# Performance work log

Measured on AMD Instinct MI355X. Metric: run time of the kernel, lower is better.

## Reference

```python
import jax, jax.numpy as jnp
import numpy as np

TAU = 10.0          # tau_init
R_MAX = 8           # max(groupconvs)
GROUPCONVS = (4, 8)
PADS = (0, 8)       # (k - spat_red)//2 for k in (17, 33), spat_red = 33 - 2*8 = 17
NEG_SLOPE = 0.01    # LeakyReLU default


def lrelu(t):
    return jnp.where(t >= 0, t, NEG_SLOPE * t)


def rotate_kernel(w, theta):
    """Rotate square kernels w:[N,k,k] by theta, matching torch
    F.affine_grid + F.grid_sample (bilinear, zero padding, align_corners=False)."""
    N, k, _ = w.shape
    coords = (2.0 * jnp.arange(k) + 1.0) / k - 1.0  # normalized pixel centers
    gy, gx = jnp.meshgrid(coords, coords, indexing='ij')
    c, s = jnp.cos(theta), jnp.sin(theta)
    sx = c * gx - s * gy
    sy = s * gx + c * gy
    fx = ((sx + 1.0) * k - 1.0) / 2.0
    fy = ((sy + 1.0) * k - 1.0) / 2.0
    x0 = jnp.floor(fx).astype(jnp.int32)
    y0 = jnp.floor(fy).astype(jnp.int32)
    wf = w.reshape(N, k * k)

    def gather(yi, xi):
        valid = ((yi >= 0) & (yi < k) & (xi >= 0) & (xi < k)).astype(w.dtype)
        idx = jnp.clip(yi, 0, k - 1) * k + jnp.clip(xi, 0, k - 1)
        return wf[:, idx.reshape(-1)].reshape(N, k, k) * valid

    wx1 = fx - x0
    wy1 = fy - y0
    return (gather(y0, x0) * (1 - wy1) * (1 - wx1)
            + gather(y0, x0 + 1) * (1 - wy1) * wx1
            + gather(y0 + 1, x0) * wy1 * (1 - wx1)
            + gather(y0 + 1, x0 + 1) * wy1 * wx1)


def group_conv(x, w, b, pad):
    """GroupConv with input_rot_dim=1: x [B,1,H,W], w [O,1,1,k,k] -> [B,O,R_MAX,H',W']."""
    O, k = w.shape[0], w.shape[-1]
    w2 = w.reshape(O, k, k)
    angles = (2.0 * jnp.pi / R_MAX) * jnp.arange(R_MAX)
    tw = jax.vmap(lambda th: rotate_kernel(w2, th))(angles)   # [R,O,k,k]
    tw = jnp.transpose(tw, (1, 0, 2, 3)).reshape(O * R_MAX, 1, k, k)
    y = jax.lax.conv_general_dilated(x, tw, (1, 1), [(pad, pad), (pad, pad)],
                                     dimension_numbers=('NCHW', 'OIHW', 'NCHW'))
    B, _, H, W = y.shape
    return y.reshape(B, O, R_MAX, H, W) + b[None, :, None, None, None]


def conv1x1(h, w, b):
    # 1x1x1 Conv3d: h [B,C,R,H,W], w [O,C], b [O]
    return jnp.einsum('bcrhw,oc->borhw', h, w) + b[None, :, None, None, None]


def scatter_sum(outs, weights, axis):
    """slice_scatter-based alignment: embed smaller-rdim tensors into the
    largest one at stride max_dim//dim, weight, and sum."""
    max_out = outs[-1]
    md = max_out.shape[axis]
    total = max_out * weights[-1]
    for i, o in enumerate(outs[:-1]):
        step = md // o.shape[axis]
        idx = tuple(slice(None, None, step) if a == axis else slice(None)
                    for a in range(max_out.ndim))
        total = total + jnp.zeros_like(max_out).at[idx].set(o) * weights[i]
    return total


OFFSETS = np.array([0, np.pi / 4, np.pi / 2, 3 * np.pi / 4, np.pi,
                    -3 * np.pi / 4, -np.pi / 2, -np.pi / 4], dtype=np.float32)


def _forward(x, ksize_weight, rdim_weight, conv1_w0, conv1_b0, conv1_w1, conv1_b1,
             conv2_w, conv2_b, conva_w, conva_b, convz_w, convz_b,
             g_ksize, g_rdim, g_attn):
    # gumbel-softmax over kernel sizes (soft, tau=TAU)
    alphas = jax.nn.softmax((ksize_weight + g_ksize) / TAU)
    x_out = (alphas[0] * lrelu(group_conv(x, conv1_w0, conv1_b0, PADS[0]))
             + alphas[1] * lrelu(group_conv(x, conv1_w1, conv1_b1, PADS[1])))
    xs_out = [x_out[:, :, ::R_MAX // r] for r in GROUPCONVS]
    hs = [lrelu(conv1x1(xo, conv2_w[i], conv2_b[i])) for i, xo in enumerate(xs_out)]
    attns = [conv1x1(h, conva_w[i], conva_b[i])[:, 0] for i, h in enumerate(hs)]
    betas = jax.nn.softmax((rdim_weight + g_rdim) / TAU)
    attn = scatter_sum(attns, betas, axis=1)          # [B,R,H,W]
    offsets = jnp.asarray(OFFSETS)
    sigma = np.pi  # theta_prior; Normal(0, sigma) log-prob at offsets
    p_r = (-0.5 * (offsets / sigma) ** 2 - np.float32(np.log(sigma))
           - np.float32(0.5 * np.log(2.0 * np.pi)))[:, None, None]
    attn = attn + p_r
    B = attn.shape[0]
    flat = attn.reshape(B, -1)
    q_t_r = jax.nn.log_softmax(flat, axis=1).reshape(attn.shape)
    # F.gumbel_softmax(a, dim=-1) with default tau=1
    a_sampled = jax.nn.softmax(flat + g_attn, axis=-1).reshape(attn.shape)
    zs = [conv1x1(h, convz_w[i], convz_b[i]) for i, h in enumerate(hs)]
    z = scatter_sum(zs, betas, axis=2)                # [B,2L,R,H,W]
    # faithful to source: `thetas = [c_r(h) for c_r, h in zip(self.conv_z, hs)]`
    # reuses conv_z, so pre-refinement theta == z
    theta_pre = z
    rotation_offset = jnp.broadcast_to(offsets[None, :, None, None], a_sampled.shape)
    theta = jnp.stack((theta_pre[:, 0] + rotation_offset, theta_pre[:, 1]), axis=1)
    return attn, q_t_r, p_r, a_sampled, offsets, theta, z


def setup_inputs() -> dict:
    key = jax.random.key(0)
    ks = jax.random.split(key, 16)
    B, n, KN, L = 8, 64, 128, 2
    gum = lambda k, shape: -jnp.log(-jnp.log(
        jax.random.uniform(k, shape, jnp.float32, 1e-10, 1.0)))
    return {
        'x': jax.random.normal(ks[0], (B, 1, n, n), jnp.float32),
        'ksize_weight': 0.001 * jax.random.normal(ks[1], (2,), jnp.float32),
        'rdim_weight': 0.001 * jax.random.normal(ks[2], (2,), jnp.float32),
        'conv1_w0': 0.02 * jax.random.normal(ks[3], (KN, 1, 1, 17, 17), jnp.float32),
        'conv1_b0': 0.01 * jax.random.normal(ks[4], (KN,), jnp.float32),
        'conv1_w1': 0.02 * jax.random.normal(ks[5], (KN, 1, 1, 33, 33), jnp.float32),
        'conv1_b1': 0.01 * jax.random.normal(ks[6], (KN,), jnp.float32),
        'conv2_w': (1.0 / np.sqrt(KN)) * jax.random.normal(ks[7], (2, KN, KN), jnp.float32),
        'conv2_b': 0.01 * jax.random.normal(ks[8], (2, KN), jnp.float32),
        'conva_w': (1.0 / np.sqrt(KN)) * jax.random.normal(ks[9], (2, 1, KN), jnp.float32),
        'conva_b': 0.01 * jax.random.normal(ks[10], (2, 1), jnp.float32),
        'convz_w': (1.0 / np.sqrt(KN)) * jax.random.normal(ks[11], (2, 2 * L, KN), jnp.float32),
        'convz_b': 0.01 * jax.random.normal(ks[12], (2, 2 * L), jnp.float32),
        'g_ksize': gum(ks[13], (2,)),
        'g_rdim': gum(ks[14], (2,)),
        'g_attn': gum(ks[15], (B, R_MAX * 48 * 48)),
    }


def reference(x, ksize_weight, rdim_weight, conv1_w0, conv1_b0, conv1_w1, conv1_b1,
              conv2_w, conv2_b, conva_w, conva_b, convz_w, convz_b,
              g_ksize, g_rdim, g_attn):
    return _forward(x, ksize_weight, rdim_weight, conv1_w0, conv1_b0, conv1_w1,
                    conv1_b1, conv2_w, conv2_b, conva_w, conva_b, convz_w, convz_b,
                    g_ksize, g_rdim, g_attn)
```

## Files before the change

### kernel.cpp

```cpp
#include <hip/hip_runtime.h>
#include <hip/hip_bf16.h>
#include <math.h>

#define PI_D 3.14159265358979323846

typedef __attribute__((ext_vector_type(8))) short bf16x8;
typedef __attribute__((ext_vector_type(4))) float f32x4;
typedef __attribute__((ext_vector_type(4))) unsigned int u32x4;

#define OFF_SCAL   0u
#define OFF_W2B    4u
#define OFF_BF     16388u
#define OFF_XOUTB  917508u
#define OFF_A0     10354692u
#define OFF_A1     10428420u
#define OFF_Z0     10575876u
#define OFF_Z1     10870788u

#define NS33 42
#define NS17 13

__device__ __forceinline__ float off_r(int r) {
  int m = (r <= 4) ? r : r - 8;
  return (float)(PI_D / 4.0) * (float)m;
}
__device__ __forceinline__ float lrelu_f(float v) { return (v >= 0.f) ? v : 0.01f * v; }
__device__ __forceinline__ short f2bf(float f) {
  __bf16 h = (__bf16)f;
  return __builtin_bit_cast(short, h);
}

__global__ void k_prep(const float* __restrict__ kw, const float* __restrict__ gk,
                       const float* __restrict__ rw, const float* __restrict__ gr,
                       const float* __restrict__ w0, const float* __restrict__ w1,
                       const float* __restrict__ w2, float* __restrict__ scal,
                       short* __restrict__ w2b, short* __restrict__ bfrag) {
  int t = blockIdx.x * blockDim.x + threadIdx.x;
  if (t == 0) {
    float a0 = (kw[0] + gk[0]) * 0.1f, a1 = (kw[1] + gk[1]) * 0.1f;
    float m = fmaxf(a0, a1);
    float e0 = expf(a0 - m), e1 = expf(a1 - m), inv = 1.f / (e0 + e1);
    scal[0] = e0 * inv; scal[1] = e1 * inv;
    float b0 = (rw[0] + gr[0]) * 0.1f, b1 = (rw[1] + gr[1]) * 0.1f;
    m = fmaxf(b0, b1);
    e0 = expf(b0 - m); e1 = expf(b1 - m); inv = 1.f / (e0 + e1);
    scal[2] = e0 * inv; scal[3] = e1 * inv;
  }
  if (t < 2 * 128 * 128) w2b[t] = f2bf(w2[t]);
  int o = t & 127;
  int q = t >> 7;
  int kb = q & 3; q >>= 2;
  int c = q % 55; int r = q / 55;
  float theta = (float)(PI_D / 4.0) * (float)r;
  float cth = cosf(theta), sth = sinf(theta);
  short out[8];
#pragma unroll
  for (int j = 0; j < 8; ++j) {
    float val = 0.f;
    int kk, k, dy, dx;
    const float* wsrc;
    if (c < NS33) { kk = 32 * c + 8 * kb + j; k = 33; dy = kk / 40; dx = kk - 40 * dy; wsrc = w1; }
    else          { kk = 32 * (c - NS33) + 8 * kb + j; k = 17; dy = kk / 24; dx = kk - 24 * dy; wsrc = w0; }
    if (dy < k && dx < k) {
      int kk2 = k * k;
      const float* wo = wsrc + o * kk2;
      float cy = (2.0f * (float)dy + 1.0f) / (float)k - 1.0f;
      float cx = (2.0f * (float)dx + 1.0f) / (float)k - 1.0f;
      float sx = cth * cx - sth * cy;
      float sy = sth * cx + cth * cy;
      float fx = ((sx + 1.0f) * (float)k - 1.0f) * 0.5f;
      float fy = ((sy + 1.0f) * (float)k - 1.0f) * 0.5f;
      float x0f = floorf(fx), y0f = floorf(fy);
      int x0 = (int)x0f, y0 = (int)y0f;
      float wx1 = fx - x0f, wy1 = fy - y0f;
      float acc = 0.f;
#define CORNER(Y, X, CW) { int yy = (Y), xx = (X); \
      if (yy >= 0 && yy < k && xx >= 0 && xx < k) acc += wo[yy * k + xx] * (CW); }
      CORNER(y0,     x0,     (1.f - wy1) * (1.f - wx1));
      CORNER(y0,     x0 + 1, (1.f - wy1) * wx1);
      CORNER(y0 + 1, x0,     wy1 * (1.f - wx1));
      CORNER(y0 + 1, x0 + 1, wy1 * wx1);
#undef CORNER
      val = acc;
    }
    out[j] = f2bf(val);
  }
  *(bf16x8*)(bfrag + (size_t)t * 8) =
      (bf16x8){out[0], out[1], out[2], out[3], out[4], out[5], out[6], out[7]};
}

#define TDW 3080
#define SHW 1544
__global__ __launch_bounds__(256, 4) void k_conv_mfma(
    const float* __restrict__ x, const short* __restrict__ bfrag,
    const float* __restrict__ b17, const float* __restrict__ b33,
    const float* __restrict__ scal, short* __restrict__ xoutb) {
  __shared__ unsigned int lds[SHW + 1540];
  unsigned short* lA = (unsigned short*)lds;
  unsigned short* lB = (unsigned short*)(lds + SHW);
  int blk = blockIdx.x;
  int pt = blk % 36; int t2 = blk / 36; int r = t2 & 7, b = t2 >> 3;
  int p0 = pt * 64;
  int ybase = p0 / 48;
  int tid = threadIdx.x;
  for (int idx = tid; idx < TDW; idx += 256) {
    int ty = idx / 88, tx = idx - ty * 88;
    int gy = ybase + ty - 8, gx = tx - 8;
    float v = 0.f;
    if (gy >= 0 && gy < 64 && gx >= 0 && gx < 64) v = x[(b * 64 + gy) * 64 + gx];
    unsigned short h = (unsigned short)f2bf(v);
    lA[idx] = h;
    if (idx > 0) lB[idx - 1] = h;
  }
  if (tid == 0) lB[TDW - 1] = 0;
  __syncthreads();

  int lane = tid & 63, w = tid >> 6;
  int wm = w >> 1, wn = w & 1;
  int kc = lane >> 4;
  int ln = lane & 15;
  int mloc[2];
#pragma unroll
  for (int mf = 0; mf < 2; ++mf) {
    int p = p0 + wm * 32 + mf + 2 * ln;
    int ym = p / 48, xm = p - ym * 48;
    mloc[mf] = (ym - ybase) * 88 + xm;
  }
  const short* bb = bfrag + (size_t)r * (55 * 4 * 128 * 8);
  int nb0 = wn * 64;

  f32x4 acc33[2][4];
#pragma unroll
  for (int mf = 0; mf < 2; ++mf)
#pragma unroll
    for (int nf = 0; nf < 4; ++nf) acc33[mf][nf] = (f32x4){0.f, 0.f, 0.f, 0.f};

#define LOADB(dst, cg)                                                          \
  {                                                                             \
    _Pragma("unroll")                                                           \
    for (int nf = 0; nf < 4; ++nf)                                              \
      dst[nf] = *(const bf16x8*)(bb + ((size_t)((cg)*4 + kc) * 128 + nb0 + nf * 16 + ln) * 8); \
  }
#define READA(dst, mf, vv)                                                      \
  {                                                                             \
    int bd_ = ((vv) >> 1) + ((mf) ? SHW : 0);                                   \
    u32x4 uv_ = {lds[bd_], lds[bd_ + 1], lds[bd_ + 2], lds[bd_ + 3]};           \
    dst = __builtin_bit_cast(bf16x8, uv_);                                      \
  }

  {
    int dxb = 8 * kc;
    int off = dxb;
    bf16x8 bc[4], bn[4];
    LOADB(bc, 0);
    for (int c = 0; c < NS33; ++c) {
      if (c + 1 < NS33) LOADB(bn, c + 1);
      bf16x8 a0, a1;
      READA(a0, 0, mloc[0] + off);
      READA(a1, 1, mloc[1] + off);
#pragma unroll
      for (int nf = 0; nf < 4; ++nf) {
        acc33[0][nf] = __builtin_amdgcn_mfma_f32_16x16x32_bf16(a0, bc[nf], acc33[0][nf], 0, 0, 0);
        acc33[1][nf] = __builtin_amdgcn_mfma_f32_16x16x32_bf16(a1, bc[nf], acc33[1][nf], 0, 0, 0);
      }
#pragma unroll
      for (int nf = 0; nf < 4; ++nf) bc[nf] = bn[nf];
      int nd = dxb + 32;
      int wr = (nd >= 40);
      dxb = wr ? nd - 40 : nd;
      off += wr ? 80 : 32;
    }
  }

  f32x4 acc17[2][4];
#pragma unroll
  for (int mf = 0; mf < 2; ++mf)
#pragma unroll
    for (int nf = 0; nf < 4; ++nf) acc17[mf][nf] = (f32x4){0.f, 0.f, 0.f, 0.f};
  {
    int t8 = 8 * kc;
    int dy0 = t8 / 24;
    int dxb = t8 - 24 * dy0;
    int off = (8 + dy0) * 88 + 8 + dxb;
    for (int c = 0; c < NS17; ++c) {
      bf16x8 bc[4];
      LOADB(bc, NS33 + c);
      bf16x8 a0, a1;
      READA(a0, 0, mloc[0] + off);
      READA(a1, 1, mloc[1] + off);
#pragma unroll
      for (int nf = 0; nf < 4; ++nf) {
        acc17[0][nf] = __builtin_amdgcn_mfma_f32_16x16x32_bf16(a0, bc[nf], acc17[0][nf], 0, 0, 0);
        acc17[1][nf] = __builtin_amdgcn_mfma_f32_16x16x32_bf16(a1, bc[nf], acc17[1][nf], 0, 0, 0);
      }
      int nd = dxb + 8;
      int wr = (nd >= 24);
      dxb = wr ? nd - 24 : nd;
      off += wr ? 160 : 96;
    }
  }
#undef LOADB
#undef READA

  float a0s = scal[0], a1s = scal[1];
  int dq = lane >> 4;
#pragma unroll
  for (int nf = 0; nf < 4; ++nf) {
    int n = nb0 + nf * 16 + ln;
    float bb17 = b17[n], bb33 = b33[n];
#pragma unroll
    for (int mf = 0; mf < 2; ++mf) {
#pragma unroll
      for (int i = 0; i < 4; ++i) {
        int m = wm * 32 + mf + 8 * dq + 2 * i;
        float v = a0s * lrelu_f(acc17[mf][nf][i] + bb17)
                + a1s * lrelu_f(acc33[mf][nf][i] + bb33);
        xoutb[((size_t)(b * 8 + r) * 2304 + p0 + m) * 128 + n] = f2bf(v);
      }
    }
  }
}

__global__ __launch_bounds__(256, 8) void k_pw_mfma(
    const short* __restrict__ xoutb, const short* __restrict__ w2b_,
    const float* __restrict__ b2_, const float* __restrict__ wa_,
    const float* __restrict__ ba_, const float* __restrict__ wz_,
    const float* __restrict__ bz_,
    float* __restrict__ a0buf, float* __restrict__ z0buf,
    float* __restrict__ a1buf, float* __restrict__ z1buf) {
  __shared__ float sA[64];
  __shared__ float sZ[4][64];
  int blk = blockIdx.x;
  int i1 = (blk >= 1152);
  int lblk = i1 ? blk - 1152 : blk;
  int nR = i1 ? 8 : 4, rstep = i1 ? 1 : 2;
  const short* w2b = w2b_ + (i1 ? 128 * 128 : 0);
  const float* b2 = b2_ + (i1 ? 128 : 0);
  const float* wa = wa_ + (i1 ? 128 : 0);
  const float* ba = ba_ + i1;
  const float* wz = wz_ + (i1 ? 512 : 0);
  const float* bz = bz_ + (i1 ? 4 : 0);
  float* attn_out = i1 ? a1buf : a0buf;
  float* z_out = i1 ? z1buf : z0buf;

  int pblk = lblk % 36;
  int t = lblk / 36;
  int rl = t % nR;
  int b = t / nR;
  int pix0 = pblk * 64;
  int tid = threadIdx.x;
  int lane = tid & 63, w = tid >> 6;
  int kc = lane >> 4, ln = lane & 15;
  int pwave = pix0 + w * 16;
  const short* arow = xoutb + ((size_t)(b * 8 + rl * rstep) * 2304 + pwave) * 128;

  f32x4 acc[8];
#pragma unroll
  for (int nf = 0; nf < 8; ++nf) acc[nf] = (f32x4){0.f, 0.f, 0.f, 0.f};
#pragma unroll
  for (int s = 0; s < 4; ++s) {
    bf16x8 a = *(const bf16x8*)(arow + ln * 128 + s * 32 + kc * 8);
#pragma unroll
    for (int nf = 0; nf < 8; ++nf) {
      bf16x8 bv = *(const bf16x8*)(w2b + (nf * 16 + ln) * 128 + s * 32 + kc * 8);
      acc[nf] = __builtin_amdgcn_mfma_f32_16x16x32_bf16(a, bv, acc[nf], 0, 0, 0);
    }
  }

  float attn_acc[4] = {0.f, 0.f, 0.f, 0.f};
  float zacc[4][4];
#pragma unroll
  for (int j = 0; j < 4; ++j)
#pragma unroll
    for (int q = 0; q < 4; ++q) zacc[j][q] = 0.f;
#pragma unroll
  for (int nf = 0; nf < 8; ++nf) {
    int n = nf * 16 + ln;
    float bb2 = b2[n];
    float wan = wa[n];
    float wz0 = wz[n], wz1 = wz[128 + n], wz2 = wz[256 + n], wz3 = wz[384 + n];
#pragma unroll
    for (int q = 0; q < 4; ++q) {
      float h = lrelu_f(acc[nf][q] + bb2);
      attn_acc[q] = fmaf(wan, h, attn_acc[q]);
      zacc[0][q] = fmaf(wz0, h, zacc[0][q]);
      zacc[1][q] = fmaf(wz1, h, zacc[1][q]);
      zacc[2][q] = fmaf(wz2, h, zacc[2][q]);
      zacc[3][q] = fmaf(wz3, h, zacc[3][q]);
    }
  }
#pragma unroll
  for (int off = 1; off < 16; off <<= 1) {
#pragma unroll
    for (int q = 0; q < 4; ++q) {
      attn_acc[q] += __shfl_xor(attn_acc[q], off);
#pragma unroll
      for (int j = 0; j < 4; ++j) zacc[j][q] += __shfl_xor(zacc[j][q], off);
    }
  }
  if (ln == 0) {
    float ba0 = ba[0];
#pragma unroll
    for (int q = 0; q < 4; ++q) {
      int px = w * 16 + kc * 4 + q;
      sA[px] = attn_acc[q] + ba0;
#pragma unroll
      for (int j = 0; j < 4; ++j) sZ[j][px] = zacc[j][q] + bz[j];
    }
  }
  __syncthreads();
  int px = tid & 63, jj = tid >> 6;
  if (jj == 0)
    attn_out[((size_t)b * nR + rl) * 2304 + pix0 + px] = sA[px];
  z_out[(((size_t)b * 4 + jj) * nR + rl) * 2304 + pix0 + px] = sZ[jj][px];
}

__global__ void k_attn_combine(const float* __restrict__ a0buf, const float* __restrict__ a1buf,
                               const float* __restrict__ scal, float* __restrict__ out0,
                               float* __restrict__ out2, float* __restrict__ out4) {
  int idx = blockIdx.x * blockDim.x + threadIdx.x;
  if (idx < 8) {
    float off = off_r(idx);
    out4[idx] = off;
    float q = off / (float)PI_D;
    out2[idx] = -0.5f * q * q - logf((float)PI_D) - 0.5f * logf(2.0f * (float)PI_D);
  }
  if (idx >= 147456) return;
  int pix = idx % 2304;
  int t = idx / 2304;
  int r = t & 7, b = t >> 3;
  float v = scal[3] * a1buf[idx];
  if (!(r & 1)) v += scal[2] * a0buf[((size_t)b * 4 + (r >> 1)) * 2304 + pix];
  float q = off_r(r) / (float)PI_D;
  v += -0.5f * q * q - logf((float)PI_D) - 0.5f * logf(2.0f * (float)PI_D);
  out0[idx] = v;
}

__global__ __launch_bounds__(1024) void k_softmax(const float* __restrict__ out0,
                                                  const float* __restrict__ g,
                                                  float* __restrict__ out1,
                                                  float* __restrict__ out3) {
  int b = blockIdx.x;
  int tid = threadIdx.x;
  const float* v = out0 + (size_t)b * 18432;
  const float* gb = g + (size_t)b * 18432;
  float vl[18], gl[18];
  float m1 = -1e30f, m2 = -1e30f;
#pragma unroll
  for (int t = 0; t < 18; ++t) {
    float vv = v[tid + (t << 10)];
    float gg = gb[tid + (t << 10)];
    vl[t] = vv;
    gl[t] = vv + gg;
    m1 = fmaxf(m1, vv);
    m2 = fmaxf(m2, gl[t]);
  }
  __shared__ float red[32];
  for (int off = 32; off > 0; off >>= 1) {
    m1 = fmaxf(m1, __shfl_xor(m1, off));
    m2 = fmaxf(m2, __shfl_xor(m2, off));
  }
  int wid = tid >> 6, lane = tid & 63;
  if (lane == 0) { red[wid] = m1; red[wid + 16] = m2; }
  __syncthreads();
  float M1 = red[0], M2 = red[16];
#pragma unroll
  for (int w = 1; w < 16; ++w) { M1 = fmaxf(M1, red[w]); M2 = fmaxf(M2, red[w + 16]); }
  __syncthreads();
  float s1 = 0.f, s2 = 0.f;
#pragma unroll
  for (int t = 0; t < 18; ++t) { s1 += expf(vl[t] - M1); s2 += expf(gl[t] - M2); }
  for (int off = 32; off > 0; off >>= 1) {
    s1 += __shfl_xor(s1, off);
    s2 += __shfl_xor(s2, off);
  }
  if (lane == 0) { red[wid] = s1; red[wid + 16] = s2; }
  __syncthreads();
  float S1 = 0.f, S2 = 0.f;
#pragma unroll
  for (int w = 0; w < 16; ++w) { S1 += red[w]; S2 += red[w + 16]; }
  float lse = M1 + logf(S1);
  float inv2 = 1.0f / S2;
  float* o1 = out1 + (size_t)b * 18432;
  float* o3 = out3 + (size_t)b * 18432;
#pragma unroll
  for (int t = 0; t < 18; ++t) {
    o1[tid + (t << 10)] = vl[t] - lse;
    o3[tid + (t << 10)] = expf(gl[t] - M2) * inv2;
  }
}

__global__ void k_ztheta(const float* __restrict__ z0buf, const float* __restrict__ z1buf,
                         const float* __restrict__ scal, float* __restrict__ out5,
                         float* __restrict__ out6) {
  int idx = blockIdx.x * blockDim.x + threadIdx.x;
  if (idx >= 589824) return;
  int pix = idx % 2304;
  int t = idx / 2304;
  int r = t & 7;
  t >>= 3;
  int c = t & 3;
  int b = t >> 2;
  float v = scal[3] * z1buf[idx];
  if (!(r & 1)) v += scal[2] * z0buf[(((size_t)b * 4 + c) * 4 + (r >> 1)) * 2304 + pix];
  out6[idx] = v;
  if (c == 0)      out5[(((size_t)b * 2 + 0) * 8 + r) * 2304 + pix] = v + off_r(r);
  else if (c == 1) out5[(((size_t)b * 2 + 1) * 8 + r) * 2304 + pix] = v;
}

extern "C" void kernel_launch(void* const* d_in, const int* in_sizes, int n_in,
                              void* d_out, int out_size, void* d_ws, size_t ws_size,
                              hipStream_t stream) {
  const float* x   = (const float*)d_in[0];
  const float* ksz = (const float*)d_in[1];
  const float* rdw = (const float*)d_in[2];
  const float* w0  = (const float*)d_in[3];
  const float* b0  = (const float*)d_in[4];
  const float* w1  = (const float*)d_in[5];
  const float* b1  = (const float*)d_in[6];
  const float* w2  = (const float*)d_in[7];
  const float* b2  = (const float*)d_in[8];
  const float* wa  = (const float*)d_in[9];
  const float* ba  = (const float*)d_in[10];
  const float* wz  = (const float*)d_in[11];
  const float* bz  = (const float*)d_in[12];
  const float* gks = (const float*)d_in[13];
  const float* grd = (const float*)d_in[14];
  const float* gat = (const float*)d_in[15];
  float* out = (float*)d_out;
  float* ws  = (float*)d_ws;

  float* scal = ws + OFF_SCAL;
  short* w2b  = (short*)(ws + OFF_W2B);
  short* bfr  = (short*)(ws + OFF_BF);
  short* xoutb = (short*)(ws + OFF_XOUTB);
  float* a0b  = ws + OFF_A0;
  float* a1b  = ws + OFF_A1;
  float* z0b  = ws + OFF_Z0;
  float* z1b  = ws + OFF_Z1;

  float* out0 = out;
  float* out1 = out + 147456;
  float* out2 = out + 294912;
  float* out3 = out + 294920;
  float* out4 = out + 442376;
  float* out5 = out + 442384;
  float* out6 = out + 737296;

  k_prep<<<880, 256, 0, stream>>>(ksz, gks, rdw, grd, w0, w1, w2, scal, w2b, bfr);
  k_conv_mfma<<<2304, 256, 0, stream>>>(x, bfr, b0, b1, scal, xoutb);
  k_pw_mfma<<<3456, 256, 0, stream>>>(xoutb, w2b, b2, wa, ba, wz, bz,
                                      a0b, z0b, a1b, z1b);
  k_attn_combine<<<576, 256, 0, stream>>>(a0b, a1b, scal, out0, out2, out4);
  k_softmax<<<8, 1024, 0, stream>>>(out0, gat, out1, out3);
  k_ztheta<<<2304, 256, 0, stream>>>(z0b, z1b, scal, out5, out6);
}
```

Measured before the change: 316.3 us.

## Transpose conv weights for coalesced rotation gathers and stage conv output through LDS

A new prep kernel first transposes the group-conv weights to position-major layout, so the rotation/bilinear gather reads consecutive channels across lanes instead of strided rows. The conv kernel's epilogue now writes results into swizzled LDS and stores them to global memory as 16-byte coalesced vectors, replacing scattered 2-byte stores. The pointwise kernel's launch bounds drop from 8 to 4 blocks per SM. The costs are one extra kernel launch, extra workspace, and an additional LDS round trip with two barriers.

```diff
diff --git a/kernel.cpp b/kernel.cpp
--- a/kernel.cpp
+++ b/kernel.cpp
@@ -9,13 +9,15 @@
 typedef __attribute__((ext_vector_type(4))) unsigned int u32x4;
 
 #define OFF_SCAL   0u
-#define OFF_W2B    4u
-#define OFF_BF     16388u
-#define OFF_XOUTB  917508u
-#define OFF_A0     10354692u
-#define OFF_A1     10428420u
-#define OFF_Z0     10575876u
-#define OFF_Z1     10870788u
+#define OFF_W0T    4u
+#define OFF_W1T    36996u
+#define OFF_W2B    176388u
+#define OFF_BF     192772u
+#define OFF_XOUTB  1093892u
+#define OFF_A0     10531076u
+#define OFF_A1     10604804u
+#define OFF_Z0     10752260u
+#define OFF_Z1     11047172u
 
 #define NS33 42
 #define NS17 13
@@ -30,13 +32,14 @@
   return __builtin_bit_cast(short, h);
 }
 
-__global__ void k_prep(const float* __restrict__ kw, const float* __restrict__ gk,
-                       const float* __restrict__ rw, const float* __restrict__ gr,
-                       const float* __restrict__ w0, const float* __restrict__ w1,
-                       const float* __restrict__ w2, float* __restrict__ scal,
-                       short* __restrict__ w2b, short* __restrict__ bfrag) {
-  int t = blockIdx.x * blockDim.x + threadIdx.x;
-  if (t == 0) {
+__global__ void k_prep1(const float* __restrict__ kw, const float* __restrict__ gk,
+                        const float* __restrict__ rw, const float* __restrict__ gr,
+                        const float* __restrict__ w0, const float* __restrict__ w1,
+                        const float* __restrict__ w2, float* __restrict__ scal,
+                        float* __restrict__ w0T, float* __restrict__ w1T,
+                        short* __restrict__ w2b) {
+  int idx = blockIdx.x * blockDim.x + threadIdx.x;
+  if (idx == 0) {
     float a0 = (kw[0] + gk[0]) * 0.1f, a1 = (kw[1] + gk[1]) * 0.1f;
     float m = fmaxf(a0, a1);
     float e0 = expf(a0 - m), e1 = expf(a1 - m), inv = 1.f / (e0 + e1);
@@ -46,7 +49,24 @@
     e0 = expf(b0 - m); e1 = expf(b1 - m); inv = 1.f / (e0 + e1);
     scal[2] = e0 * inv; scal[3] = e1 * inv;
   }
-  if (t < 2 * 128 * 128) w2b[t] = f2bf(w2[t]);
+  if (idx < 289 * 128) {
+    int o = idx & 127, pos = idx >> 7;
+    w0T[pos * 128 + o] = w0[o * 289 + pos];
+    return;
+  }
+  idx -= 289 * 128;
+  if (idx < 1089 * 128) {
+    int o = idx & 127, pos = idx >> 7;
+    w1T[pos * 128 + o] = w1[o * 1089 + pos];
+    return;
+  }
+  idx -= 1089 * 128;
+  if (idx < 2 * 128 * 128) w2b[idx] = f2bf(w2[idx]);
+}
+
+__global__ void k_prep2(const float* __restrict__ w0T, const float* __restrict__ w1T,
+                        short* __restrict__ bfrag) {
+  int t = blockIdx.x * blockDim.x + threadIdx.x;
   int o = t & 127;
   int q = t >> 7;
   int kb = q & 3; q >>= 2;
@@ -58,12 +78,10 @@
   for (int j = 0; j < 8; ++j) {
     float val = 0.f;
     int kk, k, dy, dx;
-    const float* wsrc;
-    if (c < NS33) { kk = 32 * c + 8 * kb + j; k = 33; dy = kk / 40; dx = kk - 40 * dy; wsrc = w1; }
-    else          { kk = 32 * (c - NS33) + 8 * kb + j; k = 17; dy = kk / 24; dx = kk - 24 * dy; wsrc = w0; }
+    const float* wT;
+    if (c < NS33) { kk = 32 * c + 8 * kb + j; k = 33; dy = kk / 40; dx = kk - 40 * dy; wT = w1T; }
+    else          { kk = 32 * (c - NS33) + 8 * kb + j; k = 17; dy = kk / 24; dx = kk - 24 * dy; wT = w0T; }
     if (dy < k && dx < k) {
-      int kk2 = k * k;
-      const float* wo = wsrc + o * kk2;
       float cy = (2.0f * (float)dy + 1.0f) / (float)k - 1.0f;
       float cx = (2.0f * (float)dx + 1.0f) / (float)k - 1.0f;
       float sx = cth * cx - sth * cy;
@@ -75,7 +93,7 @@
       float wx1 = fx - x0f, wy1 = fy - y0f;
       float acc = 0.f;
 #define CORNER(Y, X, CW) { int yy = (Y), xx = (X); \
-      if (yy >= 0 && yy < k && xx >= 0 && xx < k) acc += wo[yy * k + xx] * (CW); }
+      if (yy >= 0 && yy < k && xx >= 0 && xx < k) acc += wT[(yy * k + xx) * 128 + o] * (CW); }
       CORNER(y0,     x0,     (1.f - wy1) * (1.f - wx1));
       CORNER(y0,     x0 + 1, (1.f - wy1) * wx1);
       CORNER(y0 + 1, x0,     wy1 * (1.f - wx1));
@@ -95,7 +113,7 @@
     const float* __restrict__ x, const short* __restrict__ bfrag,
     const float* __restrict__ b17, const float* __restrict__ b33,
     const float* __restrict__ scal, short* __restrict__ xoutb) {
-  __shared__ unsigned int lds[SHW + 1540];
+  __shared__ __align__(16) unsigned int lds[4352];
   unsigned short* lA = (unsigned short*)lds;
   unsigned short* lB = (unsigned short*)(lds + SHW);
   int blk = blockIdx.x;
@@ -202,26 +220,40 @@
 #undef LOADB
 #undef READA
 
+  __syncthreads();
+  unsigned short* sOut = (unsigned short*)lds;
   float a0s = scal[0], a1s = scal[1];
-  int dq = lane >> 4;
 #pragma unroll
   for (int nf = 0; nf < 4; ++nf) {
     int n = nb0 + nf * 16 + ln;
     float bb17 = b17[n], bb33 = b33[n];
+    int sw = n ^ (kc << 4);
 #pragma unroll
     for (int mf = 0; mf < 2; ++mf) {
 #pragma unroll
       for (int i = 0; i < 4; ++i) {
-        int m = wm * 32 + mf + 8 * dq + 2 * i;
+        int px = wm * 32 + mf + 8 * kc + 2 * i;
         float v = a0s * lrelu_f(acc17[mf][nf][i] + bb17)
                 + a1s * lrelu_f(acc33[mf][nf][i] + bb33);
-        xoutb[((size_t)(b * 8 + r) * 2304 + p0 + m) * 128 + n] = f2bf(v);
+        sOut[px * 136 + sw] = (unsigned short)f2bf(v);
       }
     }
   }
-}
-
-__global__ __launch_bounds__(256, 8) void k_pw_mfma(
+  __syncthreads();
+  size_t gbase = ((size_t)(b * 8 + r) * 2304 + p0) * 128;
+#pragma unroll
+  for (int pass = 0; pass < 4; ++pass) {
+    int L16 = pass * 256 + tid;
+    int px = L16 >> 4, u = L16 & 15;
+    int kc3 = (px >> 3) & 3;
+    int pu = u ^ (kc3 << 1);
+    const unsigned int* lp = lds + px * 68 + pu * 4;
+    u32x4 vv = {lp[0], lp[1], lp[2], lp[3]};
+    *(u32x4*)(xoutb + gbase + (size_t)L16 * 8) = vv;
+  }
+}
+
+__global__ __launch_bounds__(256, 4) void k_pw_mfma(
     const short* __restrict__ xoutb, const short* __restrict__ w2b_,
     const float* __restrict__ b2_, const float* __restrict__ wa_,
     const float* __restrict__ ba_, const float* __restrict__ wz_,
@@ -431,6 +463,8 @@
   float* ws  = (float*)d_ws;
 
   float* scal = ws + OFF_SCAL;
+  float* w0T  = ws + OFF_W0T;
+  float* w1T  = ws + OFF_W1T;
   short* w2b  = (short*)(ws + OFF_W2B);
   short* bfr  = (short*)(ws + OFF_BF);
   short* xoutb = (short*)(ws + OFF_XOUTB);
@@ -447,7 +481,8 @@
   float* out5 = out + 442384;
   float* out6 = out + 737296;
 
-  k_prep<<<880, 256, 0, stream>>>(ksz, gks, rdw, grd, w0, w1, w2, scal, w2b, bfr);
+  k_prep1<<<817, 256, 0, stream>>>(ksz, gks, rdw, grd, w0, w1, w2, scal, w0T, w1T, w2b);
+  k_prep2<<<880, 256, 0, stream>>>(w0T, w1T, bfr);
   k_conv_mfma<<<2304, 256, 0, stream>>>(x, bfr, b0, b1, scal, xoutb);
   k_pw_mfma<<<3456, 256, 0, stream>>>(xoutb, w2b, b2, wa, ba, wz, bz,
                                       a0b, z0b, a1b, z1b);
```

Result: faster. 267.5 us (-15.4%).
